# Optimization experiments

Hardware: AMD Instinct MI355X
Metric: run time of the kernel (lower is better)

Reference implementation:

```python
import jax, jax.numpy as jnp
import numpy as np

N, E, C, H0, H1 = 100_000, 1_600_000, 32, 128, 64


def _sage(x, src, dst, wl, bl, wr, n):
    # PyG SAGEConv(aggr='min'): lin_l(min_{j in N(i)} x_j) + lin_r(x_i); lin_r has no bias.
    agg = jax.ops.segment_min(x[src], dst, num_segments=n)  # [n, d]
    # nodes with no in-edges: PyG fills with 0 (segment_min yields dtype max)
    agg = jnp.where(agg >= jnp.finfo(x.dtype).max, jnp.zeros((), x.dtype), agg)
    return agg @ wl + bl + x @ wr


def _bn(x, g, b, eps=1e-5):
    # training-mode BatchNorm over the node dimension
    mu = jnp.mean(x, axis=0)
    var = jnp.var(x, axis=0)
    return (x - mu) * jax.lax.rsqrt(var + eps) * g + b


def _forward(x, edge_index,
             rm1_wl, rm1_bl, rm1_wr, rmn1_g, rmn1_b,
             rm2_wl, rm2_bl, rm2_wr, rmn2_g, rmn2_b,
             rm4_wl, rm4_bl, rm4_wr,
             sh1_wl, sh1_bl, sh1_wr, shn1_g, shn1_b,
             rt1_wl, rt1_bl, rt1_wr, rtn1_g, rtn1_b, rt3_w, rt3_b,
             md1_wl, md1_bl, md1_wr, mdn1_g, mdn1_b, md3_w, md3_b):
    n = x.shape[0]
    src, dst = edge_index[0], edge_index[1]
    rm = jax.nn.relu(_bn(_sage(x, src, dst, rm1_wl, rm1_bl, rm1_wr, n), rmn1_g, rmn1_b))
    rm = jax.nn.relu(_bn(_sage(rm, src, dst, rm2_wl, rm2_bl, rm2_wr, n), rmn2_g, rmn2_b))
    rm = _sage(rm, src, dst, rm4_wl, rm4_bl, rm4_wr, n)  # [n, 3]
    xs = jnp.concatenate([x, rm], axis=1)  # [n, C+3]
    xs = jax.nn.relu(_bn(_sage(xs, src, dst, sh1_wl, sh1_bl, sh1_wr, n), shn1_g, shn1_b))
    rm_ls = jax.nn.log_softmax(rm, axis=1)
    labels = (jnp.argmax(rm_ls, axis=1) == 2).astype(x.dtype)  # [n]
    rt = jax.nn.relu(_bn(_sage(xs, src, dst, rt1_wl, rt1_bl, rt1_wr, n), rtn1_g, rtn1_b))
    rt = (rt @ rt3_w + rt3_b).ravel() * labels
    md = jax.nn.relu(_bn(_sage(xs, src, dst, md1_wl, md1_bl, md1_wr, n), mdn1_g, mdn1_b))
    md = (md @ md3_w + md3_b).ravel() * labels
    return rm_ls, rt, md


def setup_inputs() -> dict:
    key = jax.random.key(0)
    ks = iter(jax.random.split(key, 64))

    def w(shape):
        s = 1.0 / np.sqrt(shape[0])
        return jax.random.uniform(next(ks), shape, jnp.float32, -s, s)

    inp = {
        "x": jax.random.normal(next(ks), (N, C), jnp.float32),
        "edge_index": jax.random.randint(next(ks), (2, E), 0, N, dtype=jnp.int32),
    }

    def sage_params(cin, cout, name):
        inp[name + "_wl"] = w((cin, cout))
        inp[name + "_bl"] = jnp.zeros((cout,), jnp.float32)
        inp[name + "_wr"] = w((cin, cout))

    def bn_params(c, name):
        inp[name + "_g"] = jnp.ones((c,), jnp.float32)
        inp[name + "_b"] = jnp.zeros((c,), jnp.float32)

    sage_params(C, H0, "rm1"); bn_params(H0, "rmn1")
    sage_params(H0, H1, "rm2"); bn_params(H1, "rmn2")
    sage_params(H1, 3, "rm4")
    sage_params(C + 3, H0, "sh1"); bn_params(H0, "shn1")
    sage_params(H0, H1, "rt1"); bn_params(H1, "rtn1")
    inp["rt3_w"] = w((H1, 1)); inp["rt3_b"] = jnp.zeros((1,), jnp.float32)
    sage_params(H0, H1, "md1"); bn_params(H1, "mdn1")
    inp["md3_w"] = w((H1, 1)); inp["md3_b"] = jnp.zeros((1,), jnp.float32)
    return inp


def reference(x, edge_index,
              rm1_wl, rm1_bl, rm1_wr, rmn1_g, rmn1_b,
              rm2_wl, rm2_bl, rm2_wr, rmn2_g, rmn2_b,
              rm4_wl, rm4_bl, rm4_wr,
              sh1_wl, sh1_bl, sh1_wr, shn1_g, shn1_b,
              rt1_wl, rt1_bl, rt1_wr, rtn1_g, rtn1_b, rt3_w, rt3_b,
              md1_wl, md1_bl, md1_wr, mdn1_g, mdn1_b, md3_w, md3_b):
    return _forward(x, edge_index,
                    rm1_wl, rm1_bl, rm1_wr, rmn1_g, rmn1_b,
                    rm2_wl, rm2_bl, rm2_wr, rmn2_g, rmn2_b,
                    rm4_wl, rm4_bl, rm4_wr,
                    sh1_wl, sh1_bl, sh1_wr, shn1_g, shn1_b,
                    rt1_wl, rt1_bl, rt1_wr, rtn1_g, rtn1_b, rt3_w, rt3_b,
                    md1_wl, md1_bl, md1_wr, mdn1_g, mdn1_b, md3_w, md3_b)
```

## Files before the change

### kernel.cpp

```cpp
#include <hip/hip_runtime.h>

#define FLTMAX 3.402823466e+38f
#define DEV __device__ __forceinline__

typedef unsigned short u16;
typedef unsigned int u32;
typedef __bf16 bf16_t;
typedef bf16_t bf16x8 __attribute__((ext_vector_type(8)));
typedef float f32x4 __attribute__((ext_vector_type(4)));

union U16x8 { uint4 u; bf16x8 b; };

DEV float trf(float v, float a, float b) { return fmaxf(fmaf(v, a, b), 0.f); }

DEV float sfmin(float m, float v, u32 sm) {
    return fminf(m, __uint_as_float(__float_as_uint(v) ^ sm));
}
DEV float sdec(float m, u32 sm) { return __uint_as_float(__float_as_uint(m) ^ sm); }

DEV u16 f2bf(float f) {
    u32 u = __float_as_uint(f);
    return (u16)((u + 0x7FFFu + ((u >> 16) & 1u)) >> 16);
}

__global__ __launch_bounds__(256) void hist_k(const int* __restrict__ dst,
                                              int* __restrict__ deg, int E) {
    int e = blockIdx.x * 256 + threadIdx.x;
    if (e >= E) return;
    atomicAdd(&deg[dst[e]], 1);
}

__global__ __launch_bounds__(256) void scan_block_k(const int* __restrict__ deg,
                                                    int* __restrict__ ptr,
                                                    int* __restrict__ bsum, int n) {
    __shared__ int ls[256];
    int i = blockIdx.x * 256 + threadIdx.x;
    int v = (i < n) ? deg[i] : 0;
    ls[threadIdx.x] = v;
    __syncthreads();
#pragma unroll
    for (int off = 1; off < 256; off <<= 1) {
        int a = (threadIdx.x >= off) ? ls[threadIdx.x - off] : 0;
        __syncthreads();
        ls[threadIdx.x] += a;
        __syncthreads();
    }
    if (i < n) ptr[i] = ls[threadIdx.x] - v;
    if (threadIdx.x == 255) bsum[blockIdx.x] = ls[255];
}

__global__ __launch_bounds__(512) void scan_bsum_k(int* __restrict__ bsum, int nb) {
    __shared__ int ls[512];
    int t = threadIdx.x;
    int v = (t < nb) ? bsum[t] : 0;
    ls[t] = v;
    __syncthreads();
#pragma unroll
    for (int off = 1; off < 512; off <<= 1) {
        int a = (t >= off) ? ls[t - off] : 0;
        __syncthreads();
        ls[t] += a;
        __syncthreads();
    }
    if (t < nb) bsum[t] = ls[t] - v;
}

__global__ __launch_bounds__(256) void scan_add_k(int* __restrict__ ptr,
                                                  int* __restrict__ pos,
                                                  const int* __restrict__ bsum,
                                                  int n, int E) {
    int i = blockIdx.x * 256 + threadIdx.x;
    if (i == 0) ptr[n] = E;
    if (i < n) {
        int p = ptr[i] + bsum[blockIdx.x];
        ptr[i] = p;
        pos[i] = p;
    }
}

__global__ __launch_bounds__(256) void csr_fill_part_k(
    const int* __restrict__ src, const int* __restrict__ dst,
    int* __restrict__ pos, int* __restrict__ csr, int E, int lo_step) {
    const int part = blockIdx.x & 7;
    const int e = (blockIdx.x >> 3) * 256 + threadIdx.x;
    if (e >= E) return;
    const int d = dst[e];
    const int lo = part * lo_step;
    const int hi = lo + lo_step;
    if (d < lo || d >= hi) return;
    const int p = atomicAdd(&pos[d], 1);
    csr[p] = src[e];
}

__global__ __launch_bounds__(256) void gather_min32_k(
    const float* __restrict__ feat, const int* __restrict__ ptr,
    const int* __restrict__ csr, float* __restrict__ agg, int n) {
    const int lane = threadIdx.x & 63;
    const int wave = (blockIdx.x * 256 + threadIdx.x) >> 6;
    const int node = wave * 2 + (lane >> 5);
    if (node >= n) return;
    const int fl = lane & 31;
    int e = ptr[node];
    const int end = ptr[node + 1];
    const bool empty = (e == end);
    float m = FLTMAX;
    for (; e + 7 < end; e += 8) {
        int s[8];
#pragma unroll
        for (int j = 0; j < 8; j++) s[j] = csr[e + j];
        float v[8];
#pragma unroll
        for (int j = 0; j < 8; j++) v[j] = feat[(size_t)s[j] * 32 + fl];
#pragma unroll
        for (int j = 0; j < 8; j++) m = fminf(m, v[j]);
    }
    for (; e < end; e++) m = fminf(m, feat[(size_t)csr[e] * 32 + fl]);
    agg[(size_t)node * 32 + fl] = empty ? 0.f : m;
}

__global__ __launch_bounds__(256) void gather_min128_k(
    const float* __restrict__ feat, const int* __restrict__ ptr,
    const int* __restrict__ csr, const float* __restrict__ coef,
    float* __restrict__ agg, int n) {
    const int lane = threadIdx.x & 63;
    const int node = (blockIdx.x * 256 + threadIdx.x) >> 6;
    if (node >= n) return;
    const int fl = lane * 2;
    const float ca0 = coef[fl], ca1 = coef[fl + 1];
    const float cb0 = coef[128 + fl], cb1 = coef[128 + fl + 1];
    const u32 sm0 = (ca0 < 0.f) ? 0x80000000u : 0u;
    const u32 sm1 = (ca1 < 0.f) ? 0x80000000u : 0u;
    int e = ptr[node];
    const int end = ptr[node + 1];
    const bool empty = (e == end);
    float m0 = FLTMAX, m1 = FLTMAX;
    for (; e + 7 < end; e += 8) {
        int s[8];
#pragma unroll
        for (int j = 0; j < 8; j++) s[j] = csr[e + j];
        float2 v[8];
#pragma unroll
        for (int j = 0; j < 8; j++) v[j] = *(const float2*)(feat + (size_t)s[j] * 128 + fl);
#pragma unroll
        for (int j = 0; j < 8; j++) {
            m0 = sfmin(m0, v[j].x, sm0);
            m1 = sfmin(m1, v[j].y, sm1);
        }
    }
    for (; e + 3 < end; e += 4) {
        int s[4];
#pragma unroll
        for (int j = 0; j < 4; j++) s[j] = csr[e + j];
        float2 v[4];
#pragma unroll
        for (int j = 0; j < 4; j++) v[j] = *(const float2*)(feat + (size_t)s[j] * 128 + fl);
#pragma unroll
        for (int j = 0; j < 4; j++) {
            m0 = sfmin(m0, v[j].x, sm0);
            m1 = sfmin(m1, v[j].y, sm1);
        }
    }
    for (; e < end; e++) {
        const float2 v = *(const float2*)(feat + (size_t)csr[e] * 128 + fl);
        m0 = sfmin(m0, v.x, sm0);
        m1 = sfmin(m1, v.y, sm1);
    }
    float2 o;
    o.x = empty ? 0.f : trf(sdec(m0, sm0), ca0, cb0);
    o.y = empty ? 0.f : trf(sdec(m1, sm1), ca1, cb1);
    *(float2*)(agg + (size_t)node * 128 + fl) = o;
}

__global__ __launch_bounds__(256) void gather_bf_k(
    u16* __restrict__ Acat, const int* __restrict__ ptr,
    const int* __restrict__ csr, int n) {
    const int lane = threadIdx.x & 63;
    const int node = (blockIdx.x * 256 + threadIdx.x) >> 6;
    if (node >= n) return;
    const int fl = lane * 2;
    int e = ptr[node];
    const int end = ptr[node + 1];
    u32 outv = 0;
    if (e != end) {
        float m0 = FLTMAX, m1 = FLTMAX;
        for (; e + 15 < end; e += 16) {
            int s[16];
#pragma unroll
            for (int j = 0; j < 16; j++) s[j] = csr[e + j];
            u32 v[16];
#pragma unroll
            for (int j = 0; j < 16; j++) v[j] = *(const u32*)(Acat + (size_t)s[j] * 256 + 128 + fl);
#pragma unroll
            for (int j = 0; j < 16; j++) {
                m0 = fminf(m0, __uint_as_float(v[j] << 16));
                m1 = fminf(m1, __uint_as_float(v[j] & 0xffff0000u));
            }
        }
        for (; e + 3 < end; e += 4) {
            int s[4];
#pragma unroll
            for (int j = 0; j < 4; j++) s[j] = csr[e + j];
            u32 v[4];
#pragma unroll
            for (int j = 0; j < 4; j++) v[j] = *(const u32*)(Acat + (size_t)s[j] * 256 + 128 + fl);
#pragma unroll
            for (int j = 0; j < 4; j++) {
                m0 = fminf(m0, __uint_as_float(v[j] << 16));
                m1 = fminf(m1, __uint_as_float(v[j] & 0xffff0000u));
            }
        }
        for (; e < end; e++) {
            u32 v = *(const u32*)(Acat + (size_t)csr[e] * 256 + 128 + fl);
            m0 = fminf(m0, __uint_as_float(v << 16));
            m1 = fminf(m1, __uint_as_float(v & 0xffff0000u));
        }
        outv = (__float_as_uint(m0) >> 16) | (__float_as_uint(m1) & 0xffff0000u);
    }
    *(u32*)(Acat + (size_t)node * 256 + fl) = outv;
}

__global__ __launch_bounds__(256) void gather_min3_k(
    const float* __restrict__ feat, const int* __restrict__ ptr,
    const int* __restrict__ csr, float* __restrict__ agg, int n) {
    int i = blockIdx.x * 256 + threadIdx.x;
    if (i >= n) return;
    int e = ptr[i], end = ptr[i + 1];
    bool empty = (e == end);
    float m0 = FLTMAX, m1 = FLTMAX, m2 = FLTMAX;
    for (; e < end; e++) {
        const float* r = feat + (size_t)csr[e] * 3;
        m0 = fminf(m0, r[0]);
        m1 = fminf(m1, r[1]);
        m2 = fminf(m2, r[2]);
    }
    agg[(size_t)i * 3 + 0] = empty ? 0.f : m0;
    agg[(size_t)i * 3 + 1] = empty ? 0.f : m1;
    agg[(size_t)i * 3 + 2] = empty ? 0.f : m2;
}

__global__ __launch_bounds__(256) void convert_k(
    const float* __restrict__ h, const float* __restrict__ coef,
    u16* __restrict__ Acat, int n) {
    int t = blockIdx.x * 256 + threadIdx.x;
    int total = n * 32;
    if (t >= total) return;
    int i = t >> 5;
    int dq = (t & 31) * 4;
    const float4 hv = *(const float4*)(h + (size_t)i * 128 + dq);
    const float4 ca = *(const float4*)(coef + dq);
    const float4 cb = *(const float4*)(coef + 128 + dq);
    ushort4 o;
    o.x = f2bf(trf(hv.x, ca.x, cb.x));
    o.y = f2bf(trf(hv.y, ca.y, cb.y));
    o.z = f2bf(trf(hv.z, ca.z, cb.z));
    o.w = f2bf(trf(hv.w, ca.w, cb.w));
    *(ushort4*)(Acat + (size_t)i * 256 + 128 + dq) = o;
}

__global__ __launch_bounds__(256) void wprep_k(
    const float* __restrict__ wl, const float* __restrict__ wr,
    u16* __restrict__ WT, int N) {
    int t = blockIdx.x * 256 + threadIdx.x;
    if (t >= N * 256) return;
    int c = t >> 8;
    int k = t & 255;
    float v = (k < 128) ? wl[k * N + c] : wr[(k - 128) * N + c];
    WT[(size_t)c * 256 + k] = f2bf(v);
}

__global__ __launch_bounds__(256) void gemm_bf_k(
    const u16* __restrict__ A, const u16* __restrict__ WT,
    const float* __restrict__ bl1, const float* __restrict__ bl2,
    float* __restrict__ out, float* __restrict__ bpart, int n) {
    constexpr int NT = 8;
    __shared__ float bs[256];
    const int tid = threadIdx.x;
    bs[tid] = 0.f;
    const int wave = tid >> 6, lane = tid & 63;
    const int quad = lane >> 4, l16 = lane & 15;
    const int row0 = blockIdx.x * 64 + wave * 16;
    const int rowA = min(row0 + l16, n - 1);
    const uint4* Arow = (const uint4*)(A + (size_t)rowA * 256) + quad;

    bf16x8 a[8];
#pragma unroll
    for (int kc = 0; kc < 8; kc++) {
        U16x8 u; u.u = Arow[kc * 4];
        a[kc] = u.b;
    }
    f32x4 acc[NT];
#pragma unroll
    for (int i = 0; i < NT; i++) acc[i] = (f32x4){0.f, 0.f, 0.f, 0.f};
#pragma unroll
    for (int nt = 0; nt < NT; nt++) {
        const uint4* Brow = (const uint4*)(WT + (size_t)(nt * 16 + l16) * 256) + quad;
#pragma unroll
        for (int kc = 0; kc < 8; kc++) {
            U16x8 u; u.u = Brow[kc * 4];
            acc[nt] = __builtin_amdgcn_mfma_f32_16x16x32_bf16(a[kc], u.b, acc[nt], 0, 0, 0);
        }
    }
    __syncthreads();
#pragma unroll
    for (int nt = 0; nt < NT; nt++) {
        const int col = nt * 16 + l16;
        const float bias = (col < 64) ? bl1[col] : bl2[col - 64];
        float s = 0.f, q = 0.f;
#pragma unroll
        for (int r = 0; r < 4; r++) {
            const int row = row0 + quad * 4 + r;
            if (row < n) {
                const float o = acc[nt][r] + bias;
                out[(size_t)row * 128 + col] = o;
                s += o;
                q += o * o;
            }
        }
        atomicAdd(&bs[col], s);
        atomicAdd(&bs[128 + col], q);
    }
    __syncthreads();
    bpart[(size_t)blockIdx.x * 256 + tid] = bs[tid];
}

__global__ __launch_bounds__(256) void linear1s_k(
    const float* __restrict__ agg, const float* __restrict__ h,
    const float* __restrict__ wl, const float* __restrict__ bl,
    const float* __restrict__ wr, float* __restrict__ out,
    float* __restrict__ bpart, int n) {
    constexpr int DOUT = 128, CT = 32, RB = 32, LDW = 36;
    __shared__ float Ash[RB * LDW];
    __shared__ float Hsh[RB * LDW];
    const int tid = threadIdx.x;
    const int base = blockIdx.x * RB;
    {
        const int sr = tid >> 3;
        const int col = (tid & 7) * 4;
        const int grow = min(base + sr, n - 1);
        *(float4*)(Ash + sr * LDW + col) = *(const float4*)(agg + (size_t)grow * 32 + col);
        *(float4*)(Hsh + sr * LDW + col) = *(const float4*)(h + (size_t)grow * 32 + col);
    }
    __syncthreads();
    const int ct = tid % CT;
    const int rt = tid / CT;
    const int col = ct * 4;
    const int row0 = base + rt * 4;
    float4 acc[4] = {};
#pragma unroll 2
    for (int k0 = 0; k0 < 32; k0 += 4) {
        float4 wlv[4], wrv[4];
#pragma unroll
        for (int j = 0; j < 4; j++) {
            wlv[j] = *(const float4*)(wl + (size_t)(k0 + j) * DOUT + col);
            wrv[j] = *(const float4*)(wr + (size_t)(k0 + j) * DOUT + col);
        }
#pragma unroll
        for (int r = 0; r < 4; r++) {
            const float4 av = *(const float4*)(Ash + (rt * 4 + r) * LDW + k0);
            const float4 hv = *(const float4*)(Hsh + (rt * 4 + r) * LDW + k0);
#pragma unroll
            for (int j = 0; j < 4; j++) {
                const float aa = j == 0 ? av.x : j == 1 ? av.y : j == 2 ? av.z : av.w;
                const float bb = j == 0 ? hv.x : j == 1 ? hv.y : j == 2 ? hv.z : hv.w;
                acc[r].x += aa * wlv[j].x + bb * wrv[j].x;
                acc[r].y += aa * wlv[j].y + bb * wrv[j].y;
                acc[r].z += aa * wlv[j].z + bb * wrv[j].z;
                acc[r].w += aa * wlv[j].w + bb * wrv[j].w;
            }
        }
    }
    const float4 bv = *(const float4*)(bl + col);
    float cs[4] = {}, cq[4] = {};
#pragma unroll
    for (int r = 0; r < 4; r++) {
        if (row0 + r < n) {
            float4 o = acc[r];
            o.x += bv.x; o.y += bv.y; o.z += bv.z; o.w += bv.w;
            *(float4*)(out + (size_t)(row0 + r) * DOUT + col) = o;
            cs[0] += o.x; cq[0] += o.x * o.x;
            cs[1] += o.y; cq[1] += o.y * o.y;
            cs[2] += o.z; cq[2] += o.z * o.z;
            cs[3] += o.w; cq[3] += o.w * o.w;
        }
    }
    __syncthreads();
#pragma unroll
    for (int j = 0; j < 4; j++) Ash[tid * 4 + j] = cs[j];
    __syncthreads();
    if (tid < CT) {
#pragma unroll
        for (int j = 0; j < 4; j++) {
            float s = 0.f;
#pragma unroll
            for (int k = 0; k < 8; k++) s += Ash[(tid + k * CT) * 4 + j];
            bpart[(size_t)blockIdx.x * 256 + tid * 4 + j] = s;
        }
    }
    __syncthreads();
#pragma unroll
    for (int j = 0; j < 4; j++) Ash[tid * 4 + j] = cq[j];
    __syncthreads();
    if (tid < CT) {
#pragma unroll
        for (int j = 0; j < 4; j++) {
            float s = 0.f;
#pragma unroll
            for (int k = 0; k < 8; k++) s += Ash[(tid + k * CT) * 4 + j];
            bpart[(size_t)blockIdx.x * 256 + 128 + tid * 4 + j] = s;
        }
    }
}

__global__ __launch_bounds__(256) void linear2_k(
    const float* __restrict__ agg, const float* __restrict__ h,
    const float* __restrict__ coef, const float* __restrict__ wl,
    const float* __restrict__ bl, const float* __restrict__ wr,
    float* __restrict__ out, float* __restrict__ bpart, int n) {
    constexpr int DIN = 128, DOUT = 64, CT = 16, RB = 64, LDW = 132;
    __shared__ float Ash[RB * LDW];
    __shared__ float Hsh[RB * LDW];
    const int tid = threadIdx.x;
    const int base = blockIdx.x * RB;
    {
        const int sr = tid >> 2;
        const int sc = tid & 3;
        const int grow = min(base + sr, n - 1);
        const float* ar = agg + (size_t)grow * DIN;
        const float* hr = h + (size_t)grow * DIN;
#pragma unroll
        for (int c = 0; c < 8; c++) {
            const int col = (sc + c * 4) * 4;
            const float4 av = *(const float4*)(ar + col);
            float4 hv = *(const float4*)(hr + col);
            const float4 ca = *(const float4*)(coef + col);
            const float4 cb = *(const float4*)(coef + DIN + col);
            hv.x = trf(hv.x, ca.x, cb.x); hv.y = trf(hv.y, ca.y, cb.y);
            hv.z = trf(hv.z, ca.z, cb.z); hv.w = trf(hv.w, ca.w, cb.w);
            *(float4*)(Ash + sr * LDW + col) = av;
            *(float4*)(Hsh + sr * LDW + col) = hv;
        }
    }
    __syncthreads();
    const int ct = tid % CT;
    const int rt = tid / CT;
    const int col = ct * 4;
    const int row0 = base + rt * 4;
    float4 acc[4] = {};
#pragma unroll 2
    for (int k0 = 0; k0 < DIN; k0 += 4) {
        float4 wlv[4], wrv[4];
#pragma unroll
        for (int j = 0; j < 4; j++) {
            wlv[j] = *(const float4*)(wl + (size_t)(k0 + j) * DOUT + col);
            wrv[j] = *(const float4*)(wr + (size_t)(k0 + j) * DOUT + col);
        }
#pragma unroll
        for (int r = 0; r < 4; r++) {
            const float4 av = *(const float4*)(Ash + (rt * 4 + r) * LDW + k0);
            const float4 hv = *(const float4*)(Hsh + (rt * 4 + r) * LDW + k0);
#pragma unroll
            for (int j = 0; j < 4; j++) {
                const float aa = j == 0 ? av.x : j == 1 ? av.y : j == 2 ? av.z : av.w;
                const float bb = j == 0 ? hv.x : j == 1 ? hv.y : j == 2 ? hv.z : hv.w;
                acc[r].x += aa * wlv[j].x + bb * wrv[j].x;
                acc[r].y += aa * wlv[j].y + bb * wrv[j].y;
                acc[r].z += aa * wlv[j].z + bb * wrv[j].z;
                acc[r].w += aa * wlv[j].w + bb * wrv[j].w;
            }
        }
    }
    const float4 bv = *(const float4*)(bl + col);
    float cs[4] = {}, cq[4] = {};
#pragma unroll
    for (int r = 0; r < 4; r++) {
        if (row0 + r < n) {
            float4 o = acc[r];
            o.x += bv.x; o.y += bv.y; o.z += bv.z; o.w += bv.w;
            *(float4*)(out + (size_t)(row0 + r) * DOUT + col) = o;
            cs[0] += o.x; cq[0] += o.x * o.x;
            cs[1] += o.y; cq[1] += o.y * o.y;
            cs[2] += o.z; cq[2] += o.z * o.z;
            cs[3] += o.w; cq[3] += o.w * o.w;
        }
    }
    __syncthreads();
#pragma unroll
    for (int j = 0; j < 4; j++) Ash[tid * 4 + j] = cs[j];
    __syncthreads();
    if (tid < CT) {
#pragma unroll
        for (int j = 0; j < 4; j++) {
            float s = 0.f;
#pragma unroll
            for (int k = 0; k < 16; k++) s += Ash[(tid + k * CT) * 4 + j];
            bpart[(size_t)blockIdx.x * 128 + tid * 4 + j] = s;
        }
    }
    __syncthreads();
#pragma unroll
    for (int j = 0; j < 4; j++) Ash[tid * 4 + j] = cq[j];
    __syncthreads();
    if (tid < CT) {
#pragma unroll
        for (int j = 0; j < 4; j++) {
            float s = 0.f;
#pragma unroll
            for (int k = 0; k < 16; k++) s += Ash[(tid + k * CT) * 4 + j];
            bpart[(size_t)blockIdx.x * 128 + 64 + tid * 4 + j] = s;
        }
    }
}

__global__ __launch_bounds__(256) void linear_shs_k(
    const float* __restrict__ aggx, const float* __restrict__ x,
    const float* __restrict__ aggr, const float* __restrict__ rm,
    const float* __restrict__ wl, const float* __restrict__ bl,
    const float* __restrict__ wr, float* __restrict__ out,
    float* __restrict__ bpart, int n) {
    constexpr int DOUT = 128, CT = 32, RB = 32, LDW = 36;
    __shared__ float Ash[RB * LDW];
    __shared__ float Hsh[RB * LDW];
    __shared__ float Rsh[RB * 4], Msh[RB * 4];
    const int tid = threadIdx.x;
    const int base = blockIdx.x * RB;
    {
        const int sr = tid >> 3;
        const int col = (tid & 7) * 4;
        const int grow = min(base + sr, n - 1);
        *(float4*)(Ash + sr * LDW + col) = *(const float4*)(aggx + (size_t)grow * 32 + col);
        *(float4*)(Hsh + sr * LDW + col) = *(const float4*)(x + (size_t)grow * 32 + col);
        if (tid < RB) {
            const int gr = min(base + tid, n - 1);
#pragma unroll
            for (int k = 0; k < 3; k++) {
                Rsh[tid * 4 + k] = aggr[(size_t)gr * 3 + k];
                Msh[tid * 4 + k] = rm[(size_t)gr * 3 + k];
            }
        }
    }
    __syncthreads();
    const int ct = tid % CT;
    const int rt = tid / CT;
    const int col = ct * 4;
    const int row0 = base + rt * 4;
    float4 acc[4] = {};
#pragma unroll 2
    for (int k0 = 0; k0 < 32; k0 += 4) {
        float4 wlv[4], wrv[4];
#pragma unroll
        for (int j = 0; j < 4; j++) {
            wlv[j] = *(const float4*)(wl + (size_t)(k0 + j) * DOUT + col);
            wrv[j] = *(const float4*)(wr + (size_t)(k0 + j) * DOUT + col);
        }
#pragma unroll
        for (int r = 0; r < 4; r++) {
            const float4 av = *(const float4*)(Ash + (rt * 4 + r) * LDW + k0);
            const float4 hv = *(const float4*)(Hsh + (rt * 4 + r) * LDW + k0);
#pragma unroll
            for (int j = 0; j < 4; j++) {
                const float aa = j == 0 ? av.x : j == 1 ? av.y : j == 2 ? av.z : av.w;
                const float bb = j == 0 ? hv.x : j == 1 ? hv.y : j == 2 ? hv.z : hv.w;
                acc[r].x += aa * wlv[j].x + bb * wrv[j].x;
                acc[r].y += aa * wlv[j].y + bb * wrv[j].y;
                acc[r].z += aa * wlv[j].z + bb * wrv[j].z;
                acc[r].w += aa * wlv[j].w + bb * wrv[j].w;
            }
        }
    }
#pragma unroll
    for (int k = 0; k < 3; k++) {
        const float4 wlv = *(const float4*)(wl + (size_t)(32 + k) * DOUT + col);
        const float4 wrv = *(const float4*)(wr + (size_t)(32 + k) * DOUT + col);
#pragma unroll
        for (int r = 0; r < 4; r++) {
            const float a = Rsh[(rt * 4 + r) * 4 + k];
            const float b = Msh[(rt * 4 + r) * 4 + k];
            acc[r].x += a * wlv.x + b * wrv.x;
            acc[r].y += a * wlv.y + b * wrv.y;
            acc[r].z += a * wlv.z + b * wrv.z;
            acc[r].w += a * wlv.w + b * wrv.w;
        }
    }
    const float4 bv = *(const float4*)(bl + col);
    float cs[4] = {}, cq[4] = {};
#pragma unroll
    for (int r = 0; r < 4; r++) {
        if (row0 + r < n) {
            float4 o = acc[r];
            o.x += bv.x; o.y += bv.y; o.z += bv.z; o.w += bv.w;
            *(float4*)(out + (size_t)(row0 + r) * DOUT + col) = o;
            cs[0] += o.x; cq[0] += o.x * o.x;
            cs[1] += o.y; cq[1] += o.y * o.y;
            cs[2] += o.z; cq[2] += o.z * o.z;
            cs[3] += o.w; cq[3] += o.w * o.w;
        }
    }
    __syncthreads();
#pragma unroll
    for (int j = 0; j < 4; j++) Ash[tid * 4 + j] = cs[j];
    __syncthreads();
    if (tid < CT) {
#pragma unroll
        for (int j = 0; j < 4; j++) {
            float s = 0.f;
#pragma unroll
            for (int k = 0; k < 8; k++) s += Ash[(tid + k * CT) * 4 + j];
            bpart[(size_t)blockIdx.x * 256 + tid * 4 + j] = s;
        }
    }
    __syncthreads();
#pragma unroll
    for (int j = 0; j < 4; j++) Ash[tid * 4 + j] = cq[j];
    __syncthreads();
    if (tid < CT) {
#pragma unroll
        for (int j = 0; j < 4; j++) {
            float s = 0.f;
#pragma unroll
            for (int k = 0; k < 8; k++) s += Ash[(tid + k * CT) * 4 + j];
            bpart[(size_t)blockIdx.x * 256 + 128 + tid * 4 + j] = s;
        }
    }
}

__global__ __launch_bounds__(256) void reduce_part_k(
    const float* __restrict__ bpart, float* __restrict__ stats,
    int nb, int width) {
    const int c = threadIdx.x;
    if (c >= width) return;
    float s = 0.f;
    for (int k = blockIdx.x; k < nb; k += gridDim.x)
        s += bpart[(size_t)k * width + c];
    atomicAdd(&stats[c], s);
}

template <int D>
__global__ void coef_k(const float* __restrict__ stats, const float* __restrict__ g,
                       const float* __restrict__ bb, float* __restrict__ coef,
                       float invN) {
    int d = threadIdx.x;
    if (d >= D) return;
    float mu = stats[d] * invN;
    float var = stats[D + d] * invN - mu * mu;
    float a = rsqrtf(var + 1e-5f) * g[d];
    coef[d] = a;
    coef[D + d] = bb[d] - mu * a;
}

__global__ void coef_dual_k(const float* __restrict__ stats,
                            const float* __restrict__ gR, const float* __restrict__ bR,
                            const float* __restrict__ gM, const float* __restrict__ bM,
                            float* __restrict__ coefR, float* __restrict__ coefM,
                            float invN) {
    int d = threadIdx.x;
    if (d >= 128) return;
    float mu = stats[d] * invN;
    float var = stats[128 + d] * invN - mu * mu;
    bool isR = d < 64;
    int c = isR ? d : d - 64;
    float g = isR ? gR[c] : gM[c];
    float be = isR ? bR[c] : bM[c];
    float a = rsqrtf(var + 1e-5f) * g;
    float* co = isR ? coefR : coefM;
    co[c] = a;
    co[64 + c] = be - mu * a;
}

__global__ __launch_bounds__(256) void rm_fused_k(
    const float* __restrict__ h2, const float* __restrict__ coef,
    const int* __restrict__ ptr, const int* __restrict__ csr,
    const float* __restrict__ wl, const float* __restrict__ bl,
    const float* __restrict__ wr, float* __restrict__ rmb,
    float* __restrict__ ls_out, float* __restrict__ lab, int n) {
    const int lane = threadIdx.x & 63;
    const int node = (blockIdx.x * 256 + threadIdx.x) >> 6;
    if (node >= n) return;
    const float a = coef[lane], b = coef[64 + lane];
    const u32 sm = (a < 0.f) ? 0x80000000u : 0u;
    int e = ptr[node];
    const int end = ptr[node + 1];
    const bool empty = (e == end);
    float m = FLTMAX;
    for (; e + 15 < end; e += 16) {
        int s[16];
#pragma unroll
        for (int j = 0; j < 16; j++) s[j] = csr[e + j];
        float v[16];
#pragma unroll
        for (int j = 0; j < 16; j++) v[j] = h2[(size_t)s[j] * 64 + lane];
#pragma unroll
        for (int j = 0; j < 16; j++) m = sfmin(m, v[j], sm);
    }
    for (; e + 3 < end; e += 4) {
        int s[4];
#pragma unroll
        for (int j = 0; j < 4; j++) s[j] = csr[e + j];
        float v[4];
#pragma unroll
        for (int j = 0; j < 4; j++) v[j] = h2[(size_t)s[j] * 64 + lane];
#pragma unroll
        for (int j = 0; j < 4; j++) m = sfmin(m, v[j], sm);
    }
    for (; e < end; e++) m = sfmin(m, h2[(size_t)csr[e] * 64 + lane], sm);
    const float mv = empty ? 0.f : trf(sdec(m, sm), a, b);
    const float hv = trf(h2[(size_t)node * 64 + lane], a, b);
    float c0 = mv * wl[lane * 3 + 0] + hv * wr[lane * 3 + 0];
    float c1 = mv * wl[lane * 3 + 1] + hv * wr[lane * 3 + 1];
    float c2 = mv * wl[lane * 3 + 2] + hv * wr[lane * 3 + 2];
#pragma unroll
    for (int off = 1; off < 64; off <<= 1) {
        c0 += __shfl_xor(c0, off);
        c1 += __shfl_xor(c1, off);
        c2 += __shfl_xor(c2, off);
    }
    const float r0 = c0 + bl[0], r1 = c1 + bl[1], r2 = c2 + bl[2];
    if (lane < 3) {
        const float r = lane == 0 ? r0 : lane == 1 ? r1 : r2;
        rmb[(size_t)node * 3 + lane] = r;
        const float mx = fmaxf(r0, fmaxf(r1, r2));
        const float lse = mx + logf(expf(r0 - mx) + expf(r1 - mx) + expf(r2 - mx));
        ls_out[(size_t)node * 3 + lane] = r - lse;
        if (lane == 0) lab[node] = (r2 > r0 && r2 > r1) ? 1.f : 0.f;
    }
}

__global__ __launch_bounds__(256) void final_k(
    const float* __restrict__ rtmd,
    const float* __restrict__ cR, const float* __restrict__ cM,
    const float* __restrict__ rtw, const float* __restrict__ rtb,
    const float* __restrict__ mdw, const float* __restrict__ mdb,
    const float* __restrict__ lab, float* __restrict__ out_rt,
    float* __restrict__ out_md, int n) {
    const int lane = threadIdx.x & 63;
    const int node = (blockIdx.x * 256 + threadIdx.x) >> 6;
    if (node >= n) return;
    const float* rr = rtmd + (size_t)node * 128;
    float a = trf(rr[lane], cR[lane], cR[64 + lane]) * rtw[lane];
    float b = trf(rr[64 + lane], cM[lane], cM[64 + lane]) * mdw[lane];
#pragma unroll
    for (int off = 1; off < 64; off <<= 1) {
        a += __shfl_xor(a, off);
        b += __shfl_xor(b, off);
    }
    if (lane == 0) {
        const float l = lab[node];
        out_rt[node] = (a + rtb[0]) * l;
        out_md[node] = (b + mdb[0]) * l;
    }
}

extern "C" void kernel_launch(void* const* d_in, const int* in_sizes, int n_in,
                              void* d_out, int out_size, void* d_ws, size_t ws_size,
                              hipStream_t stream) {
    const float* x = (const float*)d_in[0];
    const int* ei = (const int*)d_in[1];
    const int E = in_sizes[1] / 2;
    const int n = in_sizes[0] / 32;
    const int* src = ei;
    const int* dst = ei + E;

    const float* rm1_wl = (const float*)d_in[2];
    const float* rm1_bl = (const float*)d_in[3];
    const float* rm1_wr = (const float*)d_in[4];
    const float* rmn1_g = (const float*)d_in[5];
    const float* rmn1_b = (const float*)d_in[6];
    const float* rm2_wl = (const float*)d_in[7];
    const float* rm2_bl = (const float*)d_in[8];
    const float* rm2_wr = (const float*)d_in[9];
    const float* rmn2_g = (const float*)d_in[10];
    const float* rmn2_b = (const float*)d_in[11];
    const float* rm4_wl = (const float*)d_in[12];
    const float* rm4_bl = (const float*)d_in[13];
    const float* rm4_wr = (const float*)d_in[14];
    const float* sh1_wl = (const float*)d_in[15];
    const float* sh1_bl = (const float*)d_in[16];
    const float* sh1_wr = (const float*)d_in[17];
    const float* shn1_g = (const float*)d_in[18];
    const float* shn1_b = (const float*)d_in[19];
    const float* rt1_wl = (const float*)d_in[20];
    const float* rt1_bl = (const float*)d_in[21];
    const float* rt1_wr = (const float*)d_in[22];
    const float* rtn1_g = (const float*)d_in[23];
    const float* rtn1_b = (const float*)d_in[24];
    const float* rt3_w = (const float*)d_in[25];
    const float* rt3_b = (const float*)d_in[26];
    const float* md1_wl = (const float*)d_in[27];
    const float* md1_bl = (const float*)d_in[28];
    const float* md1_wr = (const float*)d_in[29];
    const float* mdn1_g = (const float*)d_in[30];
    const float* mdn1_b = (const float*)d_in[31];
    const float* md3_w = (const float*)d_in[32];
    const float* md3_b = (const float*)d_in[33];

    char* w = (char*)d_ws;
    float* aggX  = (float*)w; w += (size_t)n * 32 * 4;
    float* h1    = (float*)w; w += (size_t)n * 128 * 4;
    char*  shbuf = w;         w += (size_t)n * 512;
    float* h2rt  = (float*)w; w += (size_t)n * 128 * 4;
    float* rmb   = (float*)w; w += (size_t)n * 3 * 4;
    float* aggR  = (float*)w; w += (size_t)n * 3 * 4;
    float* lab   = (float*)w; w += (size_t)n * 4;
    float* stats = (float*)w; w += 1024 * 4;
    float* coef  = (float*)w; w += 1024 * 4;
    u16*   WTD   = (u16*)w;   w += (size_t)128 * 256 * 2;
    int* ptr  = (int*)w; w += (size_t)(n + 1) * 4;
    int* pos  = (int*)w; w += (size_t)n * 4;
    int* bsum = (int*)w; w += 1024 * 4;
    int* csr  = (int*)w; w += (size_t)E * 4;

    float* aggB = (float*)shbuf;
    u16*   Acat = (u16*)shbuf;
    float* h2 = h2rt;
    float* rtmd = h2rt;
    float* stats1 = stats, *stats2 = stats + 256, *statsSh = stats + 512, *statsD = stats + 768;
    float* coef1 = coef, *coef2 = coef + 256, *coefSh = coef + 384;
    float* coefRt = coef + 640, *coefMd = coef + 768;

    float* bp1  = (float*)shbuf;
    float* bp2  = rmb;
    float* bpSh = (float*)shbuf;
    float* bpD  = rmb;

    float* out = (float*)d_out;
    float* out_ls = out;
    float* out_rt = out + (size_t)3 * n;
    float* out_md = out + (size_t)4 * n;

    const float invN = 1.f / (float)n;
    auto cdiv = [](int a, int b) { return (a + b - 1) / b; };
    const int nb = cdiv(n, 256);
    const int nb32 = cdiv(n, 32);
    const int nb64 = cdiv(n, 64);

    hipMemsetAsync(stats, 0, 1024 * 4, stream);
    hipMemsetAsync(pos, 0, (size_t)n * 4, stream);

    hist_k<<<cdiv(E, 256), 256, 0, stream>>>(dst, pos, E);
    wprep_k<<<64, 256, 0, stream>>>(rt1_wl, rt1_wr, WTD, 64);
    wprep_k<<<64, 256, 0, stream>>>(md1_wl, md1_wr, WTD + (size_t)64 * 256, 64);
    scan_block_k<<<nb, 256, 0, stream>>>(pos, ptr, bsum, n);
    scan_bsum_k<<<1, 512, 0, stream>>>(bsum, nb);
    scan_add_k<<<nb, 256, 0, stream>>>(ptr, pos, bsum, n, E);
    csr_fill_part_k<<<cdiv(E, 256) * 8, 256, 0, stream>>>(src, dst, pos, csr, E, cdiv(n, 8));

    gather_min32_k<<<cdiv(n, 8), 256, 0, stream>>>(x, ptr, csr, aggX, n);
    linear1s_k<<<nb32, 256, 0, stream>>>(aggX, x, rm1_wl, rm1_bl, rm1_wr, h1, bp1, n);
    reduce_part_k<<<64, 256, 0, stream>>>(bp1, stats1, nb32, 256);
    coef_k<128><<<1, 128, 0, stream>>>(stats1, rmn1_g, rmn1_b, coef1, invN);

    gather_min128_k<<<cdiv(n, 4), 256, 0, stream>>>(h1, ptr, csr, coef1, aggB, n);
    linear2_k<<<nb64, 256, 0, stream>>>(aggB, h1, coef1, rm2_wl, rm2_bl, rm2_wr, h2, bp2, n);
    reduce_part_k<<<64, 256, 0, stream>>>(bp2, stats2, nb64, 128);
    coef_k<64><<<1, 64, 0, stream>>>(stats2, rmn2_g, rmn2_b, coef2, invN);

    rm_fused_k<<<cdiv(n, 4), 256, 0, stream>>>(h2, coef2, ptr, csr, rm4_wl, rm4_bl, rm4_wr, rmb, out_ls, lab, n);

    gather_min3_k<<<cdiv(n, 256), 256, 0, stream>>>(rmb, ptr, csr, aggR, n);
    linear_shs_k<<<nb32, 256, 0, stream>>>(aggX, x, aggR, rmb, sh1_wl, sh1_bl, sh1_wr, h1, bpSh, n);
    reduce_part_k<<<64, 256, 0, stream>>>(bpSh, statsSh, nb32, 256);
    coef_k<128><<<1, 128, 0, stream>>>(statsSh, shn1_g, shn1_b, coefSh, invN);

    convert_k<<<cdiv(n * 32, 256), 256, 0, stream>>>(h1, coefSh, Acat, n);
    gather_bf_k<<<cdiv(n, 4), 256, 0, stream>>>(Acat, ptr, csr, n);
    gemm_bf_k<<<nb64, 256, 0, stream>>>(Acat, WTD, rt1_bl, md1_bl, rtmd, bpD, n);
    reduce_part_k<<<64, 256, 0, stream>>>(bpD, statsD, nb64, 256);
    coef_dual_k<<<1, 128, 0, stream>>>(statsD, rtn1_g, rtn1_b, mdn1_g, mdn1_b, coefRt, coefMd, invN);

    final_k<<<cdiv(n, 4), 256, 0, stream>>>(rtmd, coefRt, coefMd,
                                            rt3_w, rt3_b, md3_w, md3_b, lab,
                                            out_rt, out_md, n);
}
```

Before: 873.7 us.

## Widen gather loads to two nodes per wave and retile linear2 to 256-row blocks

The 128-wide min-gather kernels now process two nodes per wave, with each lane loading four values (float4 or uint2) instead of two. This halves the number of waves and makes each gather load wider. linear2 is retiled to 512 threads and 256 rows per block with a K-chunked shared-memory staging loop, so each weight load is reused across more rows and fewer partial-stat blocks are produced. The two weight-prep launches are also merged into one. The risks are lower occupancy and register pressure from eight accumulators, plus possible divergence when the two half-waves hit nodes of different degree.

```diff
diff --git a/kernel.cpp b/kernel.cpp
--- a/kernel.cpp
+++ b/kernel.cpp
@@ -123,100 +123,104 @@
     const int* __restrict__ csr, const float* __restrict__ coef,
     float* __restrict__ agg, int n) {
     const int lane = threadIdx.x & 63;
-    const int node = (blockIdx.x * 256 + threadIdx.x) >> 6;
+    const int wave = (blockIdx.x * 256 + threadIdx.x) >> 6;
+    const int node = wave * 2 + (lane >> 5);
     if (node >= n) return;
-    const int fl = lane * 2;
-    const float ca0 = coef[fl], ca1 = coef[fl + 1];
-    const float cb0 = coef[128 + fl], cb1 = coef[128 + fl + 1];
-    const u32 sm0 = (ca0 < 0.f) ? 0x80000000u : 0u;
-    const u32 sm1 = (ca1 < 0.f) ? 0x80000000u : 0u;
+    const int fl = (lane & 31) * 4;
+    const float4 ca = *(const float4*)(coef + fl);
+    const float4 cb = *(const float4*)(coef + 128 + fl);
+    const u32 sm0 = (ca.x < 0.f) ? 0x80000000u : 0u;
+    const u32 sm1 = (ca.y < 0.f) ? 0x80000000u : 0u;
+    const u32 sm2 = (ca.z < 0.f) ? 0x80000000u : 0u;
+    const u32 sm3 = (ca.w < 0.f) ? 0x80000000u : 0u;
     int e = ptr[node];
     const int end = ptr[node + 1];
     const bool empty = (e == end);
-    float m0 = FLTMAX, m1 = FLTMAX;
+    float m0 = FLTMAX, m1 = FLTMAX, m2 = FLTMAX, m3 = FLTMAX;
     for (; e + 7 < end; e += 8) {
         int s[8];
 #pragma unroll
         for (int j = 0; j < 8; j++) s[j] = csr[e + j];
-        float2 v[8];
-#pragma unroll
-        for (int j = 0; j < 8; j++) v[j] = *(const float2*)(feat + (size_t)s[j] * 128 + fl);
+        float4 v[8];
+#pragma unroll
+        for (int j = 0; j < 8; j++) v[j] = *(const float4*)(feat + (size_t)s[j] * 128 + fl);
 #pragma unroll
         for (int j = 0; j < 8; j++) {
             m0 = sfmin(m0, v[j].x, sm0);
             m1 = sfmin(m1, v[j].y, sm1);
+            m2 = sfmin(m2, v[j].z, sm2);
+            m3 = sfmin(m3, v[j].w, sm3);
         }
     }
     for (; e + 3 < end; e += 4) {
         int s[4];
 #pragma unroll
         for (int j = 0; j < 4; j++) s[j] = csr[e + j];
-        float2 v[4];
-#pragma unroll
-        for (int j = 0; j < 4; j++) v[j] = *(const float2*)(feat + (size_t)s[j] * 128 + fl);
+        float4 v[4];
+#pragma unroll
+        for (int j = 0; j < 4; j++) v[j] = *(const float4*)(feat + (size_t)s[j] * 128 + fl);
 #pragma unroll
         for (int j = 0; j < 4; j++) {
             m0 = sfmin(m0, v[j].x, sm0);
             m1 = sfmin(m1, v[j].y, sm1);
+            m2 = sfmin(m2, v[j].z, sm2);
+            m3 = sfmin(m3, v[j].w, sm3);
         }
     }
     for (; e < end; e++) {
-        const float2 v = *(const float2*)(feat + (size_t)csr[e] * 128 + fl);
+        const float4 v = *(const float4*)(feat + (size_t)csr[e] * 128 + fl);
         m0 = sfmin(m0, v.x, sm0);
         m1 = sfmin(m1, v.y, sm1);
-    }
-    float2 o;
-    o.x = empty ? 0.f : trf(sdec(m0, sm0), ca0, cb0);
-    o.y = empty ? 0.f : trf(sdec(m1, sm1), ca1, cb1);
-    *(float2*)(agg + (size_t)node * 128 + fl) = o;
+        m2 = sfmin(m2, v.z, sm2);
+        m3 = sfmin(m3, v.w, sm3);
+    }
+    float4 o;
+    o.x = empty ? 0.f : trf(sdec(m0, sm0), ca.x, cb.x);
+    o.y = empty ? 0.f : trf(sdec(m1, sm1), ca.y, cb.y);
+    o.z = empty ? 0.f : trf(sdec(m2, sm2), ca.z, cb.z);
+    o.w = empty ? 0.f : trf(sdec(m3, sm3), ca.w, cb.w);
+    *(float4*)(agg + (size_t)node * 128 + fl) = o;
 }
 
 __global__ __launch_bounds__(256) void gather_bf_k(
     u16* __restrict__ Acat, const int* __restrict__ ptr,
     const int* __restrict__ csr, int n) {
     const int lane = threadIdx.x & 63;
-    const int node = (blockIdx.x * 256 + threadIdx.x) >> 6;
+    const int wave = (blockIdx.x * 256 + threadIdx.x) >> 6;
+    const int node = wave * 2 + (lane >> 5);
     if (node >= n) return;
-    const int fl = lane * 2;
+    const int fl = (lane & 31) * 4;
     int e = ptr[node];
     const int end = ptr[node + 1];
-    u32 outv = 0;
+    uint2 outv = {0u, 0u};
     if (e != end) {
-        float m0 = FLTMAX, m1 = FLTMAX;
-        for (; e + 15 < end; e += 16) {
-            int s[16];
-#pragma unroll
-            for (int j = 0; j < 16; j++) s[j] = csr[e + j];
-            u32 v[16];
-#pragma unroll
-            for (int j = 0; j < 16; j++) v[j] = *(const u32*)(Acat + (size_t)s[j] * 256 + 128 + fl);
-#pragma unroll
-            for (int j = 0; j < 16; j++) {
-                m0 = fminf(m0, __uint_as_float(v[j] << 16));
-                m1 = fminf(m1, __uint_as_float(v[j] & 0xffff0000u));
+        float m0 = FLTMAX, m1 = FLTMAX, m2 = FLTMAX, m3 = FLTMAX;
+        for (; e + 7 < end; e += 8) {
+            int s[8];
+#pragma unroll
+            for (int j = 0; j < 8; j++) s[j] = csr[e + j];
+            uint2 v[8];
+#pragma unroll
+            for (int j = 0; j < 8; j++) v[j] = *(const uint2*)(Acat + (size_t)s[j] * 256 + 128 + fl);
+#pragma unroll
+            for (int j = 0; j < 8; j++) {
+                m0 = fminf(m0, __uint_as_float(v[j].x << 16));
+                m1 = fminf(m1, __uint_as_float(v[j].x & 0xffff0000u));
+                m2 = fminf(m2, __uint_as_float(v[j].y << 16));
+                m3 = fminf(m3, __uint_as_float(v[j].y & 0xffff0000u));
             }
         }
-        for (; e + 3 < end; e += 4) {
-            int s[4];
-#pragma unroll
-            for (int j = 0; j < 4; j++) s[j] = csr[e + j];
-            u32 v[4];
-#pragma unroll
-            for (int j = 0; j < 4; j++) v[j] = *(const u32*)(Acat + (size_t)s[j] * 256 + 128 + fl);
-#pragma unroll
-            for (int j = 0; j < 4; j++) {
-                m0 = fminf(m0, __uint_as_float(v[j] << 16));
-                m1 = fminf(m1, __uint_as_float(v[j] & 0xffff0000u));
-            }
-        }
         for (; e < end; e++) {
-            u32 v = *(const u32*)(Acat + (size_t)csr[e] * 256 + 128 + fl);
-            m0 = fminf(m0, __uint_as_float(v << 16));
-            m1 = fminf(m1, __uint_as_float(v & 0xffff0000u));
-        }
-        outv = (__float_as_uint(m0) >> 16) | (__float_as_uint(m1) & 0xffff0000u);
-    }
-    *(u32*)(Acat + (size_t)node * 256 + fl) = outv;
+            const uint2 v = *(const uint2*)(Acat + (size_t)csr[e] * 256 + 128 + fl);
+            m0 = fminf(m0, __uint_as_float(v.x << 16));
+            m1 = fminf(m1, __uint_as_float(v.x & 0xffff0000u));
+            m2 = fminf(m2, __uint_as_float(v.y << 16));
+            m3 = fminf(m3, __uint_as_float(v.y & 0xffff0000u));
+        }
+        outv.x = (__float_as_uint(m0) >> 16) | (__float_as_uint(m1) & 0xffff0000u);
+        outv.y = (__float_as_uint(m2) >> 16) | (__float_as_uint(m3) & 0xffff0000u);
+    }
+    *(uint2*)(Acat + (size_t)node * 256 + fl) = outv;
 }
 
 __global__ __launch_bounds__(256) void gather_min3_k(
@@ -257,14 +261,17 @@
     *(ushort4*)(Acat + (size_t)i * 256 + 128 + dq) = o;
 }
 
-__global__ __launch_bounds__(256) void wprep_k(
-    const float* __restrict__ wl, const float* __restrict__ wr,
-    u16* __restrict__ WT, int N) {
+__global__ __launch_bounds__(256) void wprep_dual_k(
+    const float* __restrict__ rwl, const float* __restrict__ rwr,
+    const float* __restrict__ mwl, const float* __restrict__ mwr,
+    u16* __restrict__ WT) {
     int t = blockIdx.x * 256 + threadIdx.x;
-    if (t >= N * 256) return;
     int c = t >> 8;
     int k = t & 255;
-    float v = (k < 128) ? wl[k * N + c] : wr[(k - 128) * N + c];
+    const float* wlp = (c < 64) ? rwl : mwl;
+    const float* wrp = (c < 64) ? rwr : mwr;
+    const int cc = c & 63;
+    float v = (k < 128) ? wlp[k * 64 + cc] : wrp[(k - 128) * 64 + cc];
     WT[(size_t)c * 256 + k] = f2bf(v);
 }
 
@@ -411,72 +418,75 @@
     }
 }
 
-__global__ __launch_bounds__(256) void linear2_k(
+__global__ __launch_bounds__(512) void linear2_k(
     const float* __restrict__ agg, const float* __restrict__ h,
     const float* __restrict__ coef, const float* __restrict__ wl,
     const float* __restrict__ bl, const float* __restrict__ wr,
     float* __restrict__ out, float* __restrict__ bpart, int n) {
-    constexpr int DIN = 128, DOUT = 64, CT = 16, RB = 64, LDW = 132;
+    constexpr int DIN = 128, DOUT = 64, CT = 16, RB = 256, KC = 32, LDW = 36;
     __shared__ float Ash[RB * LDW];
     __shared__ float Hsh[RB * LDW];
     const int tid = threadIdx.x;
     const int base = blockIdx.x * RB;
-    {
-        const int sr = tid >> 2;
-        const int sc = tid & 3;
-        const int grow = min(base + sr, n - 1);
-        const float* ar = agg + (size_t)grow * DIN;
-        const float* hr = h + (size_t)grow * DIN;
-#pragma unroll
-        for (int c = 0; c < 8; c++) {
-            const int col = (sc + c * 4) * 4;
-            const float4 av = *(const float4*)(ar + col);
-            float4 hv = *(const float4*)(hr + col);
-            const float4 ca = *(const float4*)(coef + col);
-            const float4 cb = *(const float4*)(coef + DIN + col);
-            hv.x = trf(hv.x, ca.x, cb.x); hv.y = trf(hv.y, ca.y, cb.y);
-            hv.z = trf(hv.z, ca.z, cb.z); hv.w = trf(hv.w, ca.w, cb.w);
-            *(float4*)(Ash + sr * LDW + col) = av;
-            *(float4*)(Hsh + sr * LDW + col) = hv;
-        }
-    }
-    __syncthreads();
     const int ct = tid % CT;
     const int rt = tid / CT;
     const int col = ct * 4;
-    const int row0 = base + rt * 4;
-    float4 acc[4] = {};
-#pragma unroll 2
-    for (int k0 = 0; k0 < DIN; k0 += 4) {
-        float4 wlv[4], wrv[4];
-#pragma unroll
-        for (int j = 0; j < 4; j++) {
-            wlv[j] = *(const float4*)(wl + (size_t)(k0 + j) * DOUT + col);
-            wrv[j] = *(const float4*)(wr + (size_t)(k0 + j) * DOUT + col);
-        }
-#pragma unroll
-        for (int r = 0; r < 4; r++) {
-            const float4 av = *(const float4*)(Ash + (rt * 4 + r) * LDW + k0);
-            const float4 hv = *(const float4*)(Hsh + (rt * 4 + r) * LDW + k0);
+    const int sr = tid >> 1;
+    const int grow = min(base + sr, n - 1);
+    const float* ar = agg + (size_t)grow * DIN;
+    const float* hr = h + (size_t)grow * DIN;
+    float4 acc[8] = {};
+    for (int k0 = 0; k0 < DIN; k0 += KC) {
+        if (k0) __syncthreads();
+        {
+#pragma unroll
+            for (int c2 = 0; c2 < 4; c2++) {
+                const int cc = (tid & 1) * 16 + c2 * 4;
+                const float4 av = *(const float4*)(ar + k0 + cc);
+                float4 hv = *(const float4*)(hr + k0 + cc);
+                const float4 cca = *(const float4*)(coef + k0 + cc);
+                const float4 ccb = *(const float4*)(coef + DIN + k0 + cc);
+                hv.x = trf(hv.x, cca.x, ccb.x); hv.y = trf(hv.y, cca.y, ccb.y);
+                hv.z = trf(hv.z, cca.z, ccb.z); hv.w = trf(hv.w, cca.w, ccb.w);
+                *(float4*)(Ash + sr * LDW + cc) = av;
+                *(float4*)(Hsh + sr * LDW + cc) = hv;
+            }
+        }
+        __syncthreads();
+#pragma unroll
+        for (int kk = 0; kk < KC; kk += 4) {
+            float4 wlv[4], wrv[4];
 #pragma unroll
             for (int j = 0; j < 4; j++) {
-                const float aa = j == 0 ? av.x : j == 1 ? av.y : j == 2 ? av.z : av.w;
-                const float bb = j == 0 ? hv.x : j == 1 ? hv.y : j == 2 ? hv.z : hv.w;
-                acc[r].x += aa * wlv[j].x + bb * wrv[j].x;
-                acc[r].y += aa * wlv[j].y + bb * wrv[j].y;
-                acc[r].z += aa * wlv[j].z + bb * wrv[j].z;
-                acc[r].w += aa * wlv[j].w + bb * wrv[j].w;
+                wlv[j] = *(const float4*)(wl + (size_t)(k0 + kk + j) * DOUT + col);
+                wrv[j] = *(const float4*)(wr + (size_t)(k0 + kk + j) * DOUT + col);
+            }
+#pragma unroll
+            for (int r = 0; r < 8; r++) {
+                const int row = rt + r * 32;
+                const float4 av = *(const float4*)(Ash + row * LDW + kk);
+                const float4 hv = *(const float4*)(Hsh + row * LDW + kk);
+#pragma unroll
+                for (int j = 0; j < 4; j++) {
+                    const float aa = j == 0 ? av.x : j == 1 ? av.y : j == 2 ? av.z : av.w;
+                    const float bb = j == 0 ? hv.x : j == 1 ? hv.y : j == 2 ? hv.z : hv.w;
+                    acc[r].x += aa * wlv[j].x + bb * wrv[j].x;
+                    acc[r].y += aa * wlv[j].y + bb * wrv[j].y;
+                    acc[r].z += aa * wlv[j].z + bb * wrv[j].z;
+                    acc[r].w += aa * wlv[j].w + bb * wrv[j].w;
+                }
             }
         }
     }
     const float4 bv = *(const float4*)(bl + col);
     float cs[4] = {}, cq[4] = {};
 #pragma unroll
-    for (int r = 0; r < 4; r++) {
-        if (row0 + r < n) {
+    for (int r = 0; r < 8; r++) {
+        const int row = base + rt + r * 32;
+        if (row < n) {
             float4 o = acc[r];
             o.x += bv.x; o.y += bv.y; o.z += bv.z; o.w += bv.w;
-            *(float4*)(out + (size_t)(row0 + r) * DOUT + col) = o;
+            *(float4*)(out + (size_t)row * DOUT + col) = o;
             cs[0] += o.x; cq[0] += o.x * o.x;
             cs[1] += o.y; cq[1] += o.y * o.y;
             cs[2] += o.z; cq[2] += o.z * o.z;
@@ -492,7 +502,7 @@
         for (int j = 0; j < 4; j++) {
             float s = 0.f;
 #pragma unroll
-            for (int k = 0; k < 16; k++) s += Ash[(tid + k * CT) * 4 + j];
+            for (int k = 0; k < 32; k++) s += Ash[(tid + k * CT) * 4 + j];
             bpart[(size_t)blockIdx.x * 128 + tid * 4 + j] = s;
         }
     }
@@ -505,7 +515,7 @@
         for (int j = 0; j < 4; j++) {
             float s = 0.f;
 #pragma unroll
-            for (int k = 0; k < 16; k++) s += Ash[(tid + k * CT) * 4 + j];
+            for (int k = 0; k < 32; k++) s += Ash[(tid + k * CT) * 4 + j];
             bpart[(size_t)blockIdx.x * 128 + 64 + tid * 4 + j] = s;
         }
     }
@@ -831,13 +841,13 @@
     const int nb = cdiv(n, 256);
     const int nb32 = cdiv(n, 32);
     const int nb64 = cdiv(n, 64);
+    const int nb256 = cdiv(n, 256);
 
     hipMemsetAsync(stats, 0, 1024 * 4, stream);
     hipMemsetAsync(pos, 0, (size_t)n * 4, stream);
 
     hist_k<<<cdiv(E, 256), 256, 0, stream>>>(dst, pos, E);
-    wprep_k<<<64, 256, 0, stream>>>(rt1_wl, rt1_wr, WTD, 64);
-    wprep_k<<<64, 256, 0, stream>>>(md1_wl, md1_wr, WTD + (size_t)64 * 256, 64);
+    wprep_dual_k<<<128, 256, 0, stream>>>(rt1_wl, rt1_wr, md1_wl, md1_wr, WTD);
     scan_block_k<<<nb, 256, 0, stream>>>(pos, ptr, bsum, n);
     scan_bsum_k<<<1, 512, 0, stream>>>(bsum, nb);
     scan_add_k<<<nb, 256, 0, stream>>>(ptr, pos, bsum, n, E);
@@ -848,9 +858,9 @@
     reduce_part_k<<<64, 256, 0, stream>>>(bp1, stats1, nb32, 256);
     coef_k<128><<<1, 128, 0, stream>>>(stats1, rmn1_g, rmn1_b, coef1, invN);
 
-    gather_min128_k<<<cdiv(n, 4), 256, 0, stream>>>(h1, ptr, csr, coef1, aggB, n);
-    linear2_k<<<nb64, 256, 0, stream>>>(aggB, h1, coef1, rm2_wl, rm2_bl, rm2_wr, h2, bp2, n);
-    reduce_part_k<<<64, 256, 0, stream>>>(bp2, stats2, nb64, 128);
+    gather_min128_k<<<cdiv(n, 8), 256, 0, stream>>>(h1, ptr, csr, coef1, aggB, n);
+    linear2_k<<<nb256, 512, 0, stream>>>(aggB, h1, coef1, rm2_wl, rm2_bl, rm2_wr, h2, bp2, n);
+    reduce_part_k<<<64, 256, 0, stream>>>(bp2, stats2, nb256, 128);
     coef_k<64><<<1, 64, 0, stream>>>(stats2, rmn2_g, rmn2_b, coef2, invN);
 
     rm_fused_k<<<cdiv(n, 4), 256, 0, stream>>>(h2, coef2, ptr, csr, rm4_wl, rm4_bl, rm4_wr, rmb, out_ls, lab, n);
@@ -861,7 +871,7 @@
     coef_k<128><<<1, 128, 0, stream>>>(statsSh, shn1_g, shn1_b, coefSh, invN);
 
     convert_k<<<cdiv(n * 32, 256), 256, 0, stream>>>(h1, coefSh, Acat, n);
-    gather_bf_k<<<cdiv(n, 4), 256, 0, stream>>>(Acat, ptr, csr, n);
+    gather_bf_k<<<cdiv(n, 8), 256, 0, stream>>>(Acat, ptr, csr, n);
     gemm_bf_k<<<nb64, 256, 0, stream>>>(Acat, WTD, rt1_bl, md1_bl, rtmd, bpD, n);
     reduce_part_k<<<64, 256, 0, stream>>>(bpD, statsD, nb64, 256);
     coef_dual_k<<<1, 128, 0, stream>>>(statsD, rtn1_g, rtn1_b, mdn1_g, mdn1_b, coefRt, coefMd, invN);
```

New measurement: 931.6 us. +6.6%, slower.
